# Optimization experiments

Measured on AMD Instinct MI355X. Metric: run time of the kernel, lower is better.

## Reference

```python
import math
import jax, jax.numpy as jnp
import numpy as np

B, T, C, H = 4, 2048, 1024, 16
D = C // H  # head dim = 64


def setup_inputs() -> dict:
    key = jax.random.key(0)
    ks = jax.random.split(key, 9)
    s = 1.0 / math.sqrt(C)
    return {
        "x": jax.random.normal(ks[0], (B, T, C), jnp.float32),
        "Wq": jax.random.normal(ks[1], (C, C), jnp.float32) * s,
        "bq": jax.random.normal(ks[2], (C,), jnp.float32) * 0.02,
        "Wk": jax.random.normal(ks[3], (C, C), jnp.float32) * s,
        "bk": jax.random.normal(ks[4], (C,), jnp.float32) * 0.02,
        "Wv": jax.random.normal(ks[5], (C, C), jnp.float32) * s,
        "bv": jax.random.normal(ks[6], (C,), jnp.float32) * 0.02,
        "Wo": jax.random.normal(ks[7], (C, C), jnp.float32) * s,
        "bo": jax.random.normal(ks[8], (C,), jnp.float32) * 0.02,
    }


def reference(x, Wq, bq, Wk, bk, Wv, bv, Wo, bo):
    # Projections: (B,T,C) -> (B,H,T,D)
    def heads(y):
        return y.reshape(B, T, H, D).transpose(0, 2, 1, 3)

    q = heads(x @ Wq + bq)
    k = heads(x @ Wk + bk)
    v = heads(x @ Wv + bv)

    scale = 1.0 / math.sqrt(D)
    scores = jnp.einsum("bhqd,bhkd->bhqk", q, k) * scale  # (B,H,T,T)
    causal = jnp.tril(jnp.ones((T, T), dtype=bool))
    scores = jnp.where(causal[None, None], scores, jnp.float32(-jnp.inf))
    att = jax.nn.softmax(scores, axis=-1)

    y = jnp.einsum("bhqk,bhkd->bhqd", att, v)  # (B,H,T,D)
    y = y.transpose(0, 2, 1, 3).reshape(B, T, C)
    return y @ Wo + bo
```

## Files before the change

### kernel.cpp

```cpp
#include <hip/hip_runtime.h>

#define B_ 4
#define T_ 2048
#define C_ 1024
#define H_ 16
#define D_ 64
#define M_ (B_*T_)
#define CR3 3072

typedef unsigned short u16;
typedef __attribute__((ext_vector_type(8))) short short8;
typedef __attribute__((ext_vector_type(8))) unsigned short ushort8_t;
typedef __attribute__((ext_vector_type(4))) unsigned short ushort4_t;
typedef __attribute__((ext_vector_type(4))) float floatx4;
typedef __attribute__((ext_vector_type(16))) float f32x16;
typedef __attribute__((ext_vector_type(4))) unsigned int uint4_t;

__device__ __forceinline__ u16 f2bf(float f) {
  union { float f; unsigned u; } v; v.f = f;
  unsigned r = v.u + 0x7fffu + ((v.u >> 16) & 1u);
  return (u16)(r >> 16);
}

__device__ __forceinline__ void gload16(const void* g, void* l) {
  __builtin_amdgcn_global_load_lds((__attribute__((address_space(1))) void*)(g),
                                   (__attribute__((address_space(3))) void*)(l),
                                   16, 0, 0);
}

__device__ __forceinline__ unsigned cvtpk(float lo, float hi) {
  unsigned r;
  asm("v_cvt_pk_bf16_f32 %0, %1, %2" : "=v"(r) : "v"(lo), "v"(hi));
  return r;
}

__device__ __forceinline__ void pl32swap(unsigned &a, unsigned &b) {
  asm volatile("v_permlane32_swap_b32 %0, %1" : "+v"(a), "+v"(b));
}

#define MFMA32(a, b, c) __builtin_amdgcn_mfma_f32_32x32x16_bf16(a, b, c, 0, 0, 0)
#define MFMA16(a, b, c) __builtin_amdgcn_mfma_f32_16x16x32_bf16(a, b, c, 0, 0, 0)

__global__ __launch_bounds__(256) void convx_k(const float* __restrict__ x,
                                               u16* __restrict__ o) {
  int i = (blockIdx.x * 256 + threadIdx.x) * 4;
  floatx4 v = *(const floatx4*)(x + i);
  ushort4_t r;
#pragma unroll
  for (int j = 0; j < 4; ++j) r[j] = f2bf(v[j]);
  *(ushort4_t*)(o + i) = r;
}

__global__ __launch_bounds__(256) void wconv_k(const float* __restrict__ W0,
                                               const float* __restrict__ W1,
                                               const float* __restrict__ W2,
                                               const float* __restrict__ W3,
                                               u16* __restrict__ WT) {
  __shared__ float tile[64][65];
  const float* W = blockIdx.z == 0 ? W0 : blockIdx.z == 1 ? W1 : blockIdx.z == 2 ? W2 : W3;
  const float sc = blockIdx.z == 0 ? 0.125f * 1.44269504f : 1.0f;
  u16* Wt = WT + (size_t)blockIdx.z * (C_ * C_);
  int k0 = blockIdx.x * 64, n0 = blockIdx.y * 64;
  int t = threadIdx.x;
  int r = t >> 2, c0 = (t & 3) * 16;
#pragma unroll
  for (int j = 0; j < 4; ++j) {
    floatx4 v = *(const floatx4*)(W + (size_t)(k0 + r) * C_ + n0 + c0 + j * 4);
#pragma unroll
    for (int jj = 0; jj < 4; ++jj) tile[r][c0 + j * 4 + jj] = v[jj];
  }
  __syncthreads();
  ushort8_t o0, o1;
#pragma unroll
  for (int j = 0; j < 8; ++j) o0[j] = f2bf(tile[c0 + j][r] * sc);
#pragma unroll
  for (int j = 0; j < 8; ++j) o1[j] = f2bf(tile[c0 + 8 + j][r] * sc);
  *(ushort8_t*)(Wt + (size_t)(n0 + r) * C_ + k0 + c0) = o0;
  *(ushort8_t*)(Wt + (size_t)(n0 + r) * C_ + k0 + c0 + 8) = o1;
}

__global__ __launch_bounds__(256, 2) void gemm8_k(const u16* __restrict__ A,
                                                  const u16* __restrict__ Wt,
                                                  const float* __restrict__ b0,
                                                  const float* __restrict__ b1,
                                                  const float* __restrict__ b2,
                                                  float bsc0,
                                                  u16* __restrict__ Cout) {
  __shared__ u16 lds3[36864];
  const int tid = threadIdx.x;
  const int lane = tid & 63, wn = tid >> 6;
  const int l15 = lane & 15, g = lane >> 4;

  const int bid = blockIdx.x;
  const int swz = (bid & 7) * 96 + (bid >> 3);
  const int bn = swz >> 6, bm = swz & 63;
  const int m0 = bm * 128, n0 = bn * 256;

  const int srow = tid >> 2;
  const int scol = ((tid & 3) ^ ((srow >> 1) & 3)) * 8;
  const u16* gA = A  + (size_t)(m0 + srow) * 1024 + scol;
  const u16* gB = Wt + (size_t)(n0 + srow) * 1024 + scol;

#define STAGE(KT) do { \
    u16* s_ = lds3 + ((KT) % 3) * 12288; \
    gload16(gA + (KT) * 32,                      s_ + tid * 8); \
    gload16(gA + (size_t)64 * 1024 + (KT) * 32,  s_ + 2048 + tid * 8); \
    gload16(gB + (KT) * 32,                      s_ + 4096 + tid * 8); \
    gload16(gB + (size_t)64 * 1024 + (KT) * 32,  s_ + 6144 + tid * 8); \
    gload16(gB + (size_t)128 * 1024 + (KT) * 32, s_ + 8192 + tid * 8); \
    gload16(gB + (size_t)192 * 1024 + (KT) * 32, s_ + 10240 + tid * 8); \
  } while (0)

  floatx4 acc[8][4] = {};

  STAGE(0);
  STAGE(1);

  for (int kt = 0; kt < 32; ++kt) {
    if (kt < 31) asm volatile("s_waitcnt vmcnt(6)" ::: "memory");
    else         asm volatile("s_waitcnt vmcnt(0)" ::: "memory");
    __builtin_amdgcn_s_barrier();
    __builtin_amdgcn_sched_barrier(0);
    if (kt < 30) STAGE(kt + 2);

    const u16* Ab = lds3 + (kt % 3) * 12288;
    const u16* Bb = Ab + 4096;
    short8 af[8], bf[4];
#pragma unroll
    for (int mi = 0; mi < 8; ++mi) {
      int ra = mi * 16 + l15;
      af[mi] = *(const short8*)(Ab + ra * 32 + ((g ^ ((ra >> 1) & 3)) << 3));
    }
#pragma unroll
    for (int ni = 0; ni < 4; ++ni) {
      int rb = wn * 64 + ni * 16 + l15;
      bf[ni] = *(const short8*)(Bb + rb * 32 + ((g ^ ((rb >> 1) & 3)) << 3));
    }
    __builtin_amdgcn_s_setprio(1);
#pragma unroll
    for (int mi = 0; mi < 8; ++mi)
#pragma unroll
      for (int ni = 0; ni < 4; ++ni)
        acc[mi][ni] = MFMA16(af[mi], bf[ni], acc[mi][ni]);
    __builtin_amdgcn_s_setprio(0);
  }

#pragma unroll
  for (int mi = 0; mi < 8; ++mi) {
    int row = m0 + mi * 16 + g * 4;
#pragma unroll
    for (int ni = 0; ni < 4; ++ni) {
      int col = n0 + wn * 64 + ni * 16 + l15;
      int seg = col >> 10;
      const float* bp = seg == 0 ? b0 : seg == 1 ? b1 : b2;
      float bv = bp[col & 1023] * (seg == 0 ? bsc0 : 1.0f);
#pragma unroll
      for (int i = 0; i < 4; ++i)
        Cout[(size_t)(row + i) * CR3 + col] = f2bf(acc[mi][ni][i] + bv);
    }
  }
}

__global__ __launch_bounds__(256, 2) void gemmO_k(const u16* __restrict__ A,
                                                  const u16* __restrict__ Wt,
                                                  const float* __restrict__ b0,
                                                  float* __restrict__ Cout) {
  __shared__ u16 lds3[36864];
  const int tid = threadIdx.x;
  const int lane = tid & 63, wn = tid >> 6;
  const int l15 = lane & 15, g = lane >> 4;

  const int bid = blockIdx.x;
  const int swz = (bid & 7) * 32 + (bid >> 3);
  const int bn = swz >> 6, bm = swz & 63;
  const int m0 = bm * 128, n0 = bn * 256;

  const int srow = tid >> 2;
  const int scol = ((tid & 3) ^ ((srow >> 1) & 3)) * 8;
  const u16* gA = A  + (size_t)(m0 + srow) * 1024 + scol;
  const u16* gB = Wt + (size_t)(n0 + srow) * 1024 + scol;

#define STAGEO(KT) do { \
    u16* s_ = lds3 + ((KT) % 3) * 12288; \
    gload16(gA + (KT) * 32,                      s_ + tid * 8); \
    gload16(gA + (size_t)64 * 1024 + (KT) * 32,  s_ + 2048 + tid * 8); \
    gload16(gB + (KT) * 32,                      s_ + 4096 + tid * 8); \
    gload16(gB + (size_t)64 * 1024 + (KT) * 32,  s_ + 6144 + tid * 8); \
    gload16(gB + (size_t)128 * 1024 + (KT) * 32, s_ + 8192 + tid * 8); \
    gload16(gB + (size_t)192 * 1024 + (KT) * 32, s_ + 10240 + tid * 8); \
  } while (0)

  floatx4 acc[8][4] = {};

  STAGEO(0);
  STAGEO(1);

  for (int kt = 0; kt < 32; ++kt) {
    if (kt < 31) asm volatile("s_waitcnt vmcnt(6)" ::: "memory");
    else         asm volatile("s_waitcnt vmcnt(0)" ::: "memory");
    __builtin_amdgcn_s_barrier();
    __builtin_amdgcn_sched_barrier(0);
    if (kt < 30) STAGEO(kt + 2);

    const u16* Ab = lds3 + (kt % 3) * 12288;
    const u16* Bb = Ab + 4096;
    short8 af[8], bf[4];
#pragma unroll
    for (int mi = 0; mi < 8; ++mi) {
      int ra = mi * 16 + l15;
      af[mi] = *(const short8*)(Ab + ra * 32 + ((g ^ ((ra >> 1) & 3)) << 3));
    }
#pragma unroll
    for (int ni = 0; ni < 4; ++ni) {
      int rb = wn * 64 + ni * 16 + l15;
      bf[ni] = *(const short8*)(Bb + rb * 32 + ((g ^ ((rb >> 1) & 3)) << 3));
    }
    __builtin_amdgcn_s_setprio(1);
#pragma unroll
    for (int mi = 0; mi < 8; ++mi)
#pragma unroll
      for (int ni = 0; ni < 4; ++ni)
        acc[mi][ni] = MFMA16(af[mi], bf[ni], acc[mi][ni]);
    __builtin_amdgcn_s_setprio(0);
  }

#pragma unroll
  for (int mi = 0; mi < 8; ++mi) {
    int row = m0 + mi * 16 + g * 4;
#pragma unroll
    for (int ni = 0; ni < 4; ++ni) {
      int col = n0 + wn * 64 + ni * 16 + l15;
      float bv = b0[col];
#pragma unroll
      for (int i = 0; i < 4; ++i)
        Cout[(size_t)(row + i) * 1024 + col] = acc[mi][ni][i] + bv;
    }
  }
}

__global__ __launch_bounds__(256, 2) void attn_k(const u16* __restrict__ QKV,
                                                 u16* __restrict__ Yg) {
  __shared__ u16 Ks[2][64 * 64];
  __shared__ u16 Vt[2][64 * 64];

  const int tid = threadIdx.x;
  const int w = tid >> 6, lane = tid & 63;
  const int qi = lane & 31, h = lane >> 5;

  const int lid = blockIdx.x;
  const int a4 = lid >> 6;
  const int gq = a4 >> 2, iq = a4 & 3;
  const int jt = gq == 0 ? 15 - 2 * iq : gq == 1 ? 2 * iq : gq == 2 ? 14 - 2 * iq : 1 + 2 * iq;
  const int bh = lid & 63;
  const int nt = 2 * jt + 2;

  const size_t baseQ = (size_t)(bh >> 4) * T_ * CR3 + (size_t)(bh & 15) * D_;
  const size_t baseY = (size_t)(bh >> 4) * T_ * C_ + (size_t)(bh & 15) * D_;
  const u16* Kg = QKV + baseQ + 1024;
  const u16* Vg = QKV + baseQ + 2048;

  const int srow = tid >> 3, schunk = tid & 7;
  const int sgcol = (schunk ^ (srow & 7)) * 8;
  const u16* Kgr = Kg + (size_t)srow * CR3 + sgcol;
  const u16* Vgr = Vg + (size_t)srow * CR3 + schunk * 8;

  const int qw0 = 128 * jt + 32 * w;
  const int q_abs = qw0 + qi;

  short8 qf0, qf1, qf2, qf3;
  {
    const u16* Qr = QKV + baseQ + (size_t)q_abs * CR3 + 8 * h;
    qf0 = *(const short8*)(Qr);      qf1 = *(const short8*)(Qr + 16);
    qf2 = *(const short8*)(Qr + 32); qf3 = *(const short8*)(Qr + 48);
  }

  ushort8_t va, vbr;
  gload16(Kgr, &Ks[0][tid * 8]);
  gload16(Kgr + (size_t)32 * CR3, &Ks[0][2048 + tid * 8]);
  va = *(const ushort8_t*)(Vgr);
  vbr = *(const ushort8_t*)(Vgr + (size_t)32 * CR3);

  f32x16 y0 = {}, y1 = {};
  float l_run = 0.f;
  const float M0 = 13.0f;

  for (int t = 0; t < nt; ++t) {
    const int kv0 = t * 64;
    u16* Kb = Ks[t & 1];
    u16* Vb = Vt[t & 1];
    asm volatile("s_waitcnt vmcnt(0)" ::: "memory");
    {
      char* vbp = (char*)Vb;
#pragma unroll
      for (int j = 0; j < 8; ++j) {
        int d = schunk * 8 + j;
        int sl = ((schunk ^ j) & 7) << 4;
        *(u16*)(vbp + d * 128 + ((2 * srow) ^ sl)) = va[j];
        *(u16*)(vbp + d * 128 + ((2 * (srow + 32)) ^ sl)) = vbr[j];
      }
    }
    __syncthreads();
    if (t + 1 < nt) {
      int nkv = (t + 1) * 64;
      u16* dst = Ks[(t + 1) & 1];
      gload16(Kgr + (size_t)nkv * CR3, dst + tid * 8);
      gload16(Kgr + (size_t)(nkv + 32) * CR3, dst + 2048 + tid * 8);
      va = *(const ushort8_t*)(Vgr + (size_t)nkv * CR3);
      vbr = *(const ushort8_t*)(Vgr + (size_t)(nkv + 32) * CR3);
    }

    if (kv0 <= qw0 + 31) {
      f32x16 s0 = {}, s1 = {};
      {
        const int swq = (qi & 7) << 4;
        const char* kr0 = (const char*)Kb + qi * 128;
        const char* kr1 = (const char*)Kb + (qi + 32) * 128;
        short8 k0, k1;
        k0 = *(const short8*)(kr0 + ((16 * h) ^ swq));
        k1 = *(const short8*)(kr1 + ((16 * h) ^ swq));
        __builtin_amdgcn_s_setprio(1);
        s0 = MFMA32(k0, qf0, s0); s1 = MFMA32(k1, qf0, s1);
        __builtin_amdgcn_s_setprio(0);
        k0 = *(const short8*)(kr0 + ((32 + 16 * h) ^ swq));
        k1 = *(const short8*)(kr1 + ((32 + 16 * h) ^ swq));
        __builtin_amdgcn_s_setprio(1);
        s0 = MFMA32(k0, qf1, s0); s1 = MFMA32(k1, qf1, s1);
        __builtin_amdgcn_s_setprio(0);
        k0 = *(const short8*)(kr0 + ((64 + 16 * h) ^ swq));
        k1 = *(const short8*)(kr1 + ((64 + 16 * h) ^ swq));
        __builtin_amdgcn_s_setprio(1);
        s0 = MFMA32(k0, qf2, s0); s1 = MFMA32(k1, qf2, s1);
        __builtin_amdgcn_s_setprio(0);
        k0 = *(const short8*)(kr0 + ((96 + 16 * h) ^ swq));
        k1 = *(const short8*)(kr1 + ((96 + 16 * h) ^ swq));
        __builtin_amdgcn_s_setprio(1);
        s0 = MFMA32(k0, qf3, s0); s1 = MFMA32(k1, qf3, s1);
        __builtin_amdgcn_s_setprio(0);
      }
      if (kv0 + 63 > qw0) {
#pragma unroll
        for (int r = 0; r < 16; ++r) {
          int kvq = (r & 3) + 8 * (r >> 2) + 4 * h;
          if (kv0 + kvq > q_abs) s0[r] = -1e30f;
          if (kv0 + 32 + kvq > q_abs) s1[r] = -1e30f;
        }
      }
#pragma unroll
      for (int r = 0; r < 16; ++r) s0[r] = __builtin_amdgcn_exp2f(s0[r] - M0);
#pragma unroll
      for (int r = 0; r < 16; ++r) s1[r] = __builtin_amdgcn_exp2f(s1[r] - M0);
      {
        float a8[8];
#pragma unroll
        for (int r = 0; r < 8; ++r) a8[r] = (s0[r] + s0[r + 8]) + (s1[r] + s1[r + 8]);
#pragma unroll
        for (int r = 0; r < 4; ++r) a8[r] += a8[r + 4];
        l_run += (a8[0] + a8[1]) + (a8[2] + a8[3]);
      }
      unsigned pw[16];
      {
        unsigned a0, b0, a1, b1;
        a0 = cvtpk(s0[0], s0[1]);  b0 = cvtpk(s0[4], s0[5]);  pl32swap(a0, b0);
        a1 = cvtpk(s0[2], s0[3]);  b1 = cvtpk(s0[6], s0[7]);  pl32swap(a1, b1);
        pw[0] = a0; pw[1] = a1; pw[2] = b0; pw[3] = b1;
        a0 = cvtpk(s0[8], s0[9]);  b0 = cvtpk(s0[12], s0[13]); pl32swap(a0, b0);
        a1 = cvtpk(s0[10], s0[11]); b1 = cvtpk(s0[14], s0[15]); pl32swap(a1, b1);
        pw[4] = a0; pw[5] = a1; pw[6] = b0; pw[7] = b1;
        a0 = cvtpk(s1[0], s1[1]);  b0 = cvtpk(s1[4], s1[5]);  pl32swap(a0, b0);
        a1 = cvtpk(s1[2], s1[3]);  b1 = cvtpk(s1[6], s1[7]);  pl32swap(a1, b1);
        pw[8] = a0; pw[9] = a1; pw[10] = b0; pw[11] = b1;
        a0 = cvtpk(s1[8], s1[9]);  b0 = cvtpk(s1[12], s1[13]); pl32swap(a0, b0);
        a1 = cvtpk(s1[10], s1[11]); b1 = cvtpk(s1[14], s1[15]); pl32swap(a1, b1);
        pw[12] = a0; pw[13] = a1; pw[14] = b0; pw[15] = b1;
      }
      {
        const char* vb0 = (const char*)Vb + qi * 128;
        const char* vb1 = (const char*)Vb + (qi + 32) * 128;
        const int sx0 = (((qi >> 3) ^ qi) & 7) << 4;
        const int sx1 = sx0 ^ 0x40;
#pragma unroll
        for (int c = 0; c < 4; ++c) {
          int cb = 32 * c + 16 * h;
          uint4_t pt = {pw[c * 4 + 0], pw[c * 4 + 1], pw[c * 4 + 2], pw[c * 4 + 3]};
          short8 pa = __builtin_bit_cast(short8, pt);
          short8 v0 = *(const short8*)(vb0 + (cb ^ sx0));
          short8 v1 = *(const short8*)(vb1 + (cb ^ sx1));
          __builtin_amdgcn_s_setprio(1);
          y0 = MFMA32(pa, v0, y0);
          y1 = MFMA32(pa, v1, y1);
          __builtin_amdgcn_s_setprio(0);
        }
      }
    }
  }

  l_run += __shfl_xor(l_run, 32);
  float linv = 1.0f / l_run;
#pragma unroll
  for (int r = 0; r < 16; ++r) {
    int qp = (r & 3) + 8 * (r >> 2) + 4 * h;
    float lv = __shfl(linv, qp);
    size_t row = baseY + (size_t)(qw0 + qp) * C_;
    Yg[row + qi] = f2bf(y0[r] * lv);
    Yg[row + 32 + qi] = f2bf(y1[r] * lv);
  }
}

extern "C" void kernel_launch(void* const* d_in, const int* in_sizes, int n_in,
                              void* d_out, int out_size, void* d_ws, size_t ws_size,
                              hipStream_t stream) {
  const float* x  = (const float*)d_in[0];
  const float* Wq = (const float*)d_in[1];
  const float* bq = (const float*)d_in[2];
  const float* Wk = (const float*)d_in[3];
  const float* bk = (const float*)d_in[4];
  const float* Wv = (const float*)d_in[5];
  const float* bv = (const float*)d_in[6];
  const float* Wo = (const float*)d_in[7];
  const float* bo = (const float*)d_in[8];
  float* out = (float*)d_out;

  char* ws = (char*)d_ws;
  u16* xb   = (u16*)ws;
  u16* WT   = (u16*)(ws + (size_t)16777216);
  u16* QKVb = (u16*)(ws + (size_t)25165824);
  u16* Yb = xb;

  convx_k<<<dim3(M_ * C_ / 1024), 256, 0, stream>>>(x, xb);
  wconv_k<<<dim3(16, 16, 4), 256, 0, stream>>>(Wq, Wk, Wv, Wo, WT);
  gemm8_k<<<dim3(768), 256, 0, stream>>>(xb, WT, bq, bk, bv, 0.125f * 1.44269504f, QKVb);
  attn_k<<<dim3(1024), 256, 0, stream>>>(QKVb, Yb);
  gemmO_k<<<dim3(256), 256, 0, stream>>>(Yb, WT + (size_t)3 * 1048576, bo, out);
}
```

Before: 162.9 us.

## Split long causal attention rows across two blocks and combine partials

The attention grid is rebuilt so each (batch, head) gets 24 blocks. Query tiles 0-7 are processed whole, while tiles 8-15 have their KV range split into two halves handled by separate blocks. Those split blocks write unnormalized bf16 partial outputs and row sums into scratch space reused from the output buffer and the already-consumed weight workspace. A new combine kernel adds the two halves and normalizes them. This aims to shorten the longest blocks and balance the causal workload, at the cost of an extra launch, extra scratch traffic and an extra bf16 rounding of the partials.

```diff
diff --git a/kernel.cpp b/kernel.cpp
--- a/kernel.cpp
+++ b/kernel.cpp
@@ -20,6 +20,10 @@
   union { float f; unsigned u; } v; v.f = f;
   unsigned r = v.u + 0x7fffu + ((v.u >> 16) & 1u);
   return (u16)(r >> 16);
+}
+
+__device__ __forceinline__ float bf2f(u16 x) {
+  union { unsigned u; float f; } v; v.u = ((unsigned)x) << 16; return v.f;
 }
 
 __device__ __forceinline__ void gload16(const void* g, void* l) {
@@ -239,7 +243,9 @@
 }
 
 __global__ __launch_bounds__(256, 2) void attn_k(const u16* __restrict__ QKV,
-                                                 u16* __restrict__ Yg) {
+                                                 u16* __restrict__ Yg,
+                                                 u16* __restrict__ Pscr,
+                                                 float* __restrict__ Lscr) {
   __shared__ u16 Ks[2][64 * 64];
   __shared__ u16 Vt[2][64 * 64];
 
@@ -248,11 +254,15 @@
   const int qi = lane & 31, h = lane >> 5;
 
   const int lid = blockIdx.x;
-  const int a4 = lid >> 6;
-  const int gq = a4 >> 2, iq = a4 & 3;
-  const int jt = gq == 0 ? 15 - 2 * iq : gq == 1 ? 2 * iq : gq == 2 ? 14 - 2 * iq : 1 + 2 * iq;
-  const int bh = lid & 63;
-  const int nt = 2 * jt + 2;
+  const int s = lid % 24, bh = lid / 24;
+  int jt, t0, t1, half;
+  if (s < 8) { jt = s; t0 = 0; t1 = 2 * s + 2; half = -1; }
+  else {
+    jt = 8 + ((s - 8) >> 1);
+    half = (s - 8) & 1;
+    t0 = half ? (jt + 1) : 0;
+    t1 = half ? (2 * jt + 2) : (jt + 1);
+  }
 
   const size_t baseQ = (size_t)(bh >> 4) * T_ * CR3 + (size_t)(bh & 15) * D_;
   const size_t baseY = (size_t)(bh >> 4) * T_ * C_ + (size_t)(bh & 15) * D_;
@@ -275,16 +285,20 @@
   }
 
   ushort8_t va, vbr;
-  gload16(Kgr, &Ks[0][tid * 8]);
-  gload16(Kgr + (size_t)32 * CR3, &Ks[0][2048 + tid * 8]);
-  va = *(const ushort8_t*)(Vgr);
-  vbr = *(const ushort8_t*)(Vgr + (size_t)32 * CR3);
+  {
+    int kv0 = t0 * 64;
+    u16* dst = Ks[t0 & 1];
+    gload16(Kgr + (size_t)kv0 * CR3, dst + tid * 8);
+    gload16(Kgr + (size_t)(kv0 + 32) * CR3, dst + 2048 + tid * 8);
+    va = *(const ushort8_t*)(Vgr + (size_t)kv0 * CR3);
+    vbr = *(const ushort8_t*)(Vgr + (size_t)(kv0 + 32) * CR3);
+  }
 
   f32x16 y0 = {}, y1 = {};
   float l_run = 0.f;
   const float M0 = 13.0f;
 
-  for (int t = 0; t < nt; ++t) {
+  for (int t = t0; t < t1; ++t) {
     const int kv0 = t * 64;
     u16* Kb = Ks[t & 1];
     u16* Vb = Vt[t & 1];
@@ -300,7 +314,7 @@
       }
     }
     __syncthreads();
-    if (t + 1 < nt) {
+    if (t + 1 < t1) {
       int nkv = (t + 1) * 64;
       u16* dst = Ks[(t + 1) & 1];
       gload16(Kgr + (size_t)nkv * CR3, dst + tid * 8);
@@ -395,15 +409,47 @@
   }
 
   l_run += __shfl_xor(l_run, 32);
-  float linv = 1.0f / l_run;
-#pragma unroll
-  for (int r = 0; r < 16; ++r) {
-    int qp = (r & 3) + 8 * (r >> 2) + 4 * h;
-    float lv = __shfl(linv, qp);
-    size_t row = baseY + (size_t)(qw0 + qp) * C_;
-    Yg[row + qi] = f2bf(y0[r] * lv);
-    Yg[row + 32 + qi] = f2bf(y1[r] * lv);
-  }
+  if (half < 0) {
+    float linv = 1.0f / l_run;
+#pragma unroll
+    for (int r = 0; r < 16; ++r) {
+      int qp = (r & 3) + 8 * (r >> 2) + 4 * h;
+      float lv = __shfl(linv, qp);
+      size_t row = baseY + (size_t)(qw0 + qp) * C_;
+      Yg[row + qi] = f2bf(y0[r] * lv);
+      Yg[row + 32 + qi] = f2bf(y1[r] * lv);
+    }
+  } else {
+    const int rt = (bh * 8 + (jt - 8)) * 128 + 32 * w;
+    u16* P = Pscr + (size_t)half * (64 * 8 * 128 * 64) + (size_t)rt * 64;
+#pragma unroll
+    for (int r = 0; r < 16; ++r) {
+      int qp = (r & 3) + 8 * (r >> 2) + 4 * h;
+      P[qp * 64 + qi] = f2bf(y0[r]);
+      P[qp * 64 + 32 + qi] = f2bf(y1[r]);
+    }
+    if (h == 0) Lscr[half * 65536 + rt + qi] = l_run;
+  }
+}
+
+__global__ __launch_bounds__(256) void comb_k(const u16* __restrict__ Pscr,
+                                              const float* __restrict__ Lscr,
+                                              u16* __restrict__ Yg) {
+  int idx = blockIdx.x * 256 + threadIdx.x;
+  int rg = idx >> 3, d0 = (idx & 7) * 8;
+  float inv = 1.0f / (Lscr[rg] + Lscr[65536 + rg]);
+  const u16* p0 = Pscr + (size_t)rg * 64 + d0;
+  const u16* p1 = p0 + (size_t)(64 * 8 * 128 * 64);
+  ushort8_t a = *(const ushort8_t*)p0;
+  ushort8_t b = *(const ushort8_t*)p1;
+  ushort8_t o;
+#pragma unroll
+  for (int j = 0; j < 8; ++j) o[j] = f2bf((bf2f(a[j]) + bf2f(b[j])) * inv);
+  int bh = rg >> 10, rem = rg & 1023;
+  int jt8 = rem >> 7, row = rem & 127;
+  size_t off = (size_t)(bh >> 4) * T_ * C_ + (size_t)(128 * (8 + jt8) + row) * C_
+             + (size_t)(bh & 15) * D_ + d0;
+  *(ushort8_t*)(Yg + off) = o;
 }
 
 extern "C" void kernel_launch(void* const* d_in, const int* in_sizes, int n_in,
@@ -425,10 +471,13 @@
   u16* WT   = (u16*)(ws + (size_t)16777216);
   u16* QKVb = (u16*)(ws + (size_t)25165824);
   u16* Yb = xb;
+  u16* Pscr = (u16*)d_out;
+  float* Lscr = (float*)WT;
 
   convx_k<<<dim3(M_ * C_ / 1024), 256, 0, stream>>>(x, xb);
   wconv_k<<<dim3(16, 16, 4), 256, 0, stream>>>(Wq, Wk, Wv, Wo, WT);
   gemm8_k<<<dim3(768), 256, 0, stream>>>(xb, WT, bq, bk, bv, 0.125f * 1.44269504f, QKVb);
-  attn_k<<<dim3(1024), 256, 0, stream>>>(QKVb, Yb);
+  attn_k<<<dim3(1536), 256, 0, stream>>>(QKVb, Yb, Pscr, Lscr);
+  comb_k<<<dim3(2048), 256, 0, stream>>>(Pscr, Lscr, Yb);
   gemmO_k<<<dim3(256), 256, 0, stream>>>(Yb, WT + (size_t)3 * 1048576, bo, out);
 }
```

Measured after the change: 182.6 us. 12.1% more time.
